# Optimization experiments

Measured on AMD Instinct MI355X. Metric: run time of the kernel, lower is better.

## Reference

```python
import jax, jax.numpy as jnp
import numpy as np

EPS = 1e-5
HEADS = 8  # heads kwarg of TransformerDecoder


def _ln(x, g, b):
    mu = jnp.mean(x, axis=-1, keepdims=True)
    var = jnp.var(x, axis=-1, keepdims=True)
    return (x - mu) * jax.lax.rsqrt(var + EPS) * g + b


def _expert(params, xt, m, scale):
    """One TransformerDecoder expert (BIT-style): per layer, PreNorm2 cross-attn + residual,
    then PreNorm FeedForward + residual. xt: (B,S,D), m: (B,Nt,D)."""
    an_g, an_b, wq, wk, wv, wo, wo_b, fn_g, fn_b, w1, b1, w2, b2 = params
    L = an_g.shape[0]
    B, S, D = xt.shape
    Nt = m.shape[1]
    for l in range(L):
        xn = _ln(xt, an_g[l], an_b[l])
        mn = _ln(m, an_g[l], an_b[l])  # PreNorm2 norms both streams with the same LN
        q = (xn @ wq[l]).reshape(B, S, HEADS, -1)
        k = (mn @ wk[l]).reshape(B, Nt, HEADS, -1)
        v = (mn @ wv[l]).reshape(B, Nt, HEADS, -1)
        attn = jax.nn.softmax(jnp.einsum('bihd,bjhd->bhij', q, k) * scale, axis=-1)
        o = jnp.einsum('bhij,bjhd->bihd', attn, v).reshape(B, S, -1)
        xt = xt + o @ wo[l] + wo_b[l]
        h = _ln(xt, fn_g[l], fn_b[l])
        xt = xt + jax.nn.gelu(h @ w1[l] + b1[l], approximate=False) @ w2[l] + b2[l]
    return xt


def setup_inputs():
    key = jax.random.key(0)
    ks = iter(jax.random.split(key, 40))
    B, C, H, W = 4, 128, 64, 64
    D, INNER, FF, P, L, NT = 256, 512, 1024, 4, 2, 8
    r = lambda shape, s=1.0: jax.random.normal(next(ks), shape, jnp.float32) * s
    return {
        'x': r((B, C, H, W)),
        'm': r((B, NT, D)),
        'proj_w': r((C, D), 0.05), 'proj_b': r((D,), 0.02),
        'lnp_g': jnp.ones((D,), jnp.float32), 'lnp_b': jnp.zeros((D,), jnp.float32),
        'sq_w': r((D, D), 0.05), 'sq_b': r((D,), 0.02),
        'sk_w': r((D, D), 0.05), 'sk_b': r((D,), 0.02),
        'sv_w': r((D, 1), 0.05), 'sv_b': r((1,), 0.02),
        'an_g': jnp.ones((P, L, D), jnp.float32), 'an_b': jnp.zeros((P, L, D), jnp.float32),
        'wq': r((P, L, D, INNER), 0.05), 'wk': r((P, L, D, INNER), 0.05), 'wv': r((P, L, D, INNER), 0.05),
        'wo': r((P, L, INNER, D), 0.05), 'wo_b': r((P, L, D), 0.02),
        'fn_g': jnp.ones((P, L, D), jnp.float32), 'fn_b': jnp.zeros((P, L, D), jnp.float32),
        'w1': r((P, L, D, FF), 0.05), 'b1': r((P, L, FF), 0.02),
        'w2': r((P, L, FF, D), 0.05), 'b2': r((P, L, D), 0.02),
        'fln_g': jnp.ones((D,), jnp.float32), 'fln_b': jnp.zeros((D,), jnp.float32),
    }


def reference(x, m, proj_w, proj_b, lnp_g, lnp_b, sq_w, sq_b, sk_w, sk_b, sv_w, sv_b,
              an_g, an_b, wq, wk, wv, wo, wo_b, fn_g, fn_b, w1, b1, w2, b2, fln_g, fln_b):
    B, C, H, W = x.shape
    D = proj_w.shape[1]
    # 1x1 conv -> flatten(2).transpose(1,2): row-major (h,w) tokens
    tokens = jnp.einsum('bchw,cd->bhwd', x, proj_w).reshape(B, H * W, D) + proj_b
    tokens = _ln(tokens, lnp_g, lnp_b)
    # TokenScorer: cross-attention importance scores, v projects to scalar
    q = tokens @ sq_w + sq_b
    k = m @ sk_w + sk_b
    v = m @ sv_w + sv_b  # (B, Nt, 1)
    aw = jax.nn.softmax(jnp.einsum('bnd,bmd->bnm', q, k) / jnp.sqrt(jnp.float32(D)), axis=-1)
    scores = jnp.einsum('bnm,bmo->bno', aw, v)[..., 0]  # (B, N)
    P = an_g.shape[0]
    N = tokens.shape[1]
    S = N // P
    # descending sort of token scores
    idx = jnp.argsort(-scores, axis=1)  # (B, N)
    pscores = jnp.take_along_axis(scores, idx, axis=1).reshape(B, P, S).mean(-1)  # (B, P)
    pw = jax.nn.softmax(pscores, axis=1)  # (B, P)
    # gather tokens per partition: (P, B, S, D)
    gathered = jnp.take_along_axis(tokens, idx[..., None], axis=1).reshape(B, P, S, D).transpose(1, 0, 2, 3)
    scale = 1.0 / jnp.sqrt(jnp.float32(D))  # Cross_Attention scale = dim ** -0.5
    params = (an_g, an_b, wq, wk, wv, wo, wo_b, fn_g, fn_b, w1, b1, w2, b2)
    proc = jax.vmap(lambda pr, xt: _expert(pr, xt, m, scale))(params, gathered)  # (P, B, S, D)
    proc = proc * pw.T[:, :, None, None]
    flat = proc.transpose(1, 0, 2, 3).reshape(B, N, D)
    # scatter back into original token order (idx is a permutation)
    out = jnp.zeros_like(tokens).at[jnp.arange(B)[:, None], idx].set(flat)
    return _ln(out, fln_g, fln_b)
```

## Files before the change

### kernel.cpp

```cpp
#include <hip/hip_runtime.h>
#include <hip/hip_bf16.h>
#include <math.h>

#define BB 4
#define CC 128
#define NN 4096
#define DD 256
#define INNER 512
#define FFD 1024
#define PP 4
#define LL 2
#define NT 8
#define SS 1024
#define SCALE 0.0625f

typedef __attribute__((ext_vector_type(8))) short bf16x8;
typedef __attribute__((ext_vector_type(8))) short short8;
typedef __attribute__((ext_vector_type(4))) short short4v;
typedef __attribute__((ext_vector_type(4))) float f32x4;

#define GLD_LDS16(g, l) __builtin_amdgcn_global_load_lds( \
    (const __attribute__((address_space(1))) void*)(g), \
    (__attribute__((address_space(3))) void*)(l), 16, 0, 0)

template<int NW>
__device__ inline float block_sum(float v, float* sbuf){
  #pragma unroll
  for (int mk=32; mk; mk>>=1) v += __shfl_xor(v, mk);
  int w = threadIdx.x>>6;
  if ((threadIdx.x&63)==0) sbuf[w]=v;
  __syncthreads();
  float r = 0.f;
  #pragma unroll
  for (int k=0;k<NW;k++) r += sbuf[k];
  __syncthreads();
  return r;
}

__device__ inline unsigned short bf16bits(float v){
  __hip_bfloat16 t = __float2bfloat16(v);
  unsigned short u;
  __builtin_memcpy(&u, &t, 2);
  return u;
}
__device__ inline float bf2f(unsigned short u){
  unsigned int x = ((unsigned int)u)<<16;
  float f;
  __builtin_memcpy(&f, &x, 4);
  return f;
}

__device__ inline float gelu_f(float x){
  float z  = x * 0.70710678118654752440f;
  float az = fabsf(z);
  float t  = 1.0f / (1.0f + 0.3275911f*az);
  float y  = t*(0.254829592f + t*(-0.284496736f + t*(1.421413741f +
             t*(-1.453152027f + t*1.061405429f))));
  float erfv = 1.0f - y*__expf(-az*az);
  erfv = (z < 0.0f) ? -erfv : erfv;
  return 0.5f*x*(1.0f+erfv);
}

__global__ __launch_bounds__(256) void scorer_kernel(
    const float* __restrict__ m, const float* __restrict__ sk_w,
    const float* __restrict__ sk_b, const float* __restrict__ sv_w,
    const float* __restrict__ sv_b, const float* __restrict__ sq_w,
    const float* __restrict__ sq_b,
    float* __restrict__ kk2, float* __restrict__ kb, float* __restrict__ vsc)
{
  __shared__ float ms[256];
  __shared__ float ks[256];
  __shared__ float sbuf[4];
  int bj = blockIdx.x;
  int tid = threadIdx.x;
  ms[tid] = m[bj*DD + tid];
  __syncthreads();
  float acc=0.f;
  #pragma unroll 8
  for(int c=0;c<DD;c++) acc = fmaf(ms[c], sk_w[c*DD + tid], acc);
  ks[tid] = acc + sk_b[tid];
  float sv = block_sum<4>(ms[tid]*sv_w[tid], sbuf);
  if(tid==0) vsc[bj] = sv + sv_b[0];
  __syncthreads();
  const float* wr = sq_w + (long)tid*DD;
  float a2 = 0.f;
  #pragma unroll 4
  for (int c=0; c<DD; c+=4){
    float4 wvv = *(const float4*)(wr + c);
    a2 = fmaf(wvv.x, ks[c+0], fmaf(wvv.y, ks[c+1], fmaf(wvv.z, ks[c+2], fmaf(wvv.w, ks[c+3], a2))));
  }
  kk2[bj*DD + tid] = a2;
  float kbv = block_sum<4>(sq_b[tid]*ks[tid], sbuf);
  if (tid==0) kb[bj] = kbv;
}

__global__ __launch_bounds__(256) void proj_prep_kernel(
    const float* __restrict__ x, const float* __restrict__ proj_w,
    const float* __restrict__ proj_b, const float* __restrict__ lnp_g,
    const float* __restrict__ lnp_b, const float* __restrict__ kk2,
    const float* __restrict__ kb, const float* __restrict__ vsc,
    float* __restrict__ tokens, float* __restrict__ scores,
    int* __restrict__ rank, long long* __restrict__ psumsI,
    const float* __restrict__ m, const float* __restrict__ an_g,
    const float* __restrict__ an_b, const float* __restrict__ wk,
    const float* __restrict__ wv, float* __restrict__ kvk,
    float* __restrict__ kvv,
    const float* __restrict__ wq, const float* __restrict__ w1,
    const float* __restrict__ w2,
    __hip_bfloat16* __restrict__ wqT, __hip_bfloat16* __restrict__ w1T,
    __hip_bfloat16* __restrict__ w2T)
{
  __shared__ union {
    struct {
      float ys[16][260];
      float kj[8][260];
      float kbs[8], vs[8], mu_s[16], rs_s[16];
      float lg[16][8];
    } pr;
    struct { float t[64][65]; } wc;
    struct { float mn[256]; float sbuf[4]; } kv;
  } sm;
  int z = blockIdx.x;
  int tid = threadIdx.x;

  if (z < 256){
    float* mn = sm.kv.mn;
    float* sbuf = sm.kv.sbuf;
    int idx = z;
    int j = idx & 7, b = (idx>>3)&3, pl = idx>>5;
    float v = m[(b*NT+j)*DD + tid];
    float s = block_sum<4>(v, sbuf);
    float mu = s*(1.0f/256.0f);
    float dv = v-mu;
    float q = block_sum<4>(dv*dv, sbuf);
    float rs = rsqrtf(q*(1.0f/256.0f)+1e-5f);
    mn[tid] = dv*rs*an_g[pl*DD+tid] + an_b[pl*DD+tid];
    __syncthreads();
    float ka0=0.f, va0=0.f, ka1=0.f, va1=0.f;
    const float* wkb = wk + (long)pl*DD*INNER;
    const float* wvb = wv + (long)pl*DD*INNER;
    #pragma unroll 8
    for (int c=0;c<DD;c++){
      float mc = mn[c];
      const float* wkr = wkb + (long)c*INNER;
      const float* wvr = wvb + (long)c*INNER;
      ka0 = fmaf(mc, wkr[tid], ka0);
      ka1 = fmaf(mc, wkr[tid+256], ka1);
      va0 = fmaf(mc, wvr[tid], va0);
      va1 = fmaf(mc, wvr[tid+256], va1);
    }
    long off = ((long)pl*BB + b)*(NT*INNER) + j*INNER;
    kvk[off+tid]=ka0; kvk[off+tid+256]=ka1;
    kvv[off+tid]=va0; kvv[off+tid+256]=va1;
  } else if (z < 1536){
    int z2 = z - 256;
    const float* src; __hip_bfloat16* dst; int K, N, rel;
    if (z2 < 256)      { src=wq; dst=wqT; K=DD;   N=INNER; rel=z2; }
    else if (z2 < 768) { src=w1; dst=w1T; K=DD;   N=FFD;   rel=z2-256; }
    else               { src=w2; dst=w2T; K=FFD;  N=DD;    rel=z2-768; }
    int tn = N>>6, tk = K>>6, per = tn*tk;
    int pl = rel/per, r2 = rel%per;
    int n0 = (r2%tn)*64, k0 = (r2/tn)*64;
    float (*t)[65] = sm.wc.t;
    #pragma unroll
    for (int i=0;i<4;i++){
      int idx = i*256+tid;
      int kk = idx>>4, n4 = idx&15;
      float4 v = *(const float4*)&src[((long)pl*K + k0+kk)*N + n0 + n4*4];
      t[kk][n4*4+0]=v.x; t[kk][n4*4+1]=v.y; t[kk][n4*4+2]=v.z; t[kk][n4*4+3]=v.w;
    }
    __syncthreads();
    #pragma unroll
    for (int i=0;i<4;i++){
      int idx = i*256+tid;
      int nn = idx>>4, k4 = idx&15;
      short4v o;
      o[0] = (short)bf16bits(t[k4*4+0][nn]);
      o[1] = (short)bf16bits(t[k4*4+1][nn]);
      o[2] = (short)bf16bits(t[k4*4+2][nn]);
      o[3] = (short)bf16bits(t[k4*4+3][nn]);
      *(short4v*)&dst[((long)pl*N + n0+nn)*K + k0 + k4*4] = o;
    }
  } else {
    int zz = z - 1536;
    int b  = zz >> 8;
    int n0 = (zz & 255) * 16;
    if (tid < 16) rank[b*NN + n0 + tid] = 0;
    if (zz == 0 && tid < 16) psumsI[tid] = 0;
    float (*ys)[260] = sm.pr.ys;
    float (*kj)[260] = sm.pr.kj;
    float* kbs = sm.pr.kbs; float* vs = sm.pr.vs;
    float* mu_s = sm.pr.mu_s; float* rs_s = sm.pr.rs_s;
    float (*lg)[8] = sm.pr.lg;
    #pragma unroll
    for (int i=0;i<8;i++){
      int idx = i*256 + tid;
      int r = idx >> 8, c = idx & 255;
      kj[r][c] = kk2[(b*NT + r)*DD + c];
    }
    if (tid < 8){ kbs[tid] = kb[b*NT+tid]; vs[tid] = vsc[b*NT+tid]; }
    float acc[16];
    #pragma unroll
    for (int t=0;t<16;t++) acc[t]=0.f;
    const float* xb = x + (long)(b*CC)*NN + n0;
    for (int c0=0;c0<CC;c0+=4){
      float w0 = proj_w[(c0+0)*DD + tid];
      float w1_ = proj_w[(c0+1)*DD + tid];
      float w2_ = proj_w[(c0+2)*DD + tid];
      float w3_ = proj_w[(c0+3)*DD + tid];
      const float* x0 = xb + (long)(c0+0)*NN;
      const float* x1 = xb + (long)(c0+1)*NN;
      const float* x2 = xb + (long)(c0+2)*NN;
      const float* x3 = xb + (long)(c0+3)*NN;
      #pragma unroll
      for (int t=0;t<16;t++){
        acc[t] = fmaf(x0[t],w0,fmaf(x1[t],w1_,fmaf(x2[t],w2_,fmaf(x3[t],w3_,acc[t]))));
      }
    }
    float pb = proj_b[tid];
    #pragma unroll
    for (int t=0;t<16;t++) ys[t][tid] = acc[t] + pb;
    __syncthreads();
    int w = tid>>6, lane = tid&63;
    for (int k=0;k<4;k++){
      int t = w*4+k;
      float s = ys[t][lane] + ys[t][lane+64] + ys[t][lane+128] + ys[t][lane+192];
      #pragma unroll
      for (int mk=32; mk; mk>>=1) s += __shfl_xor(s, mk);
      float mu = s*(1.0f/256.0f);
      float d0=ys[t][lane]-mu, d1=ys[t][lane+64]-mu, d2=ys[t][lane+128]-mu, d3=ys[t][lane+192]-mu;
      float q = d0*d0+d1*d1+d2*d2+d3*d3;
      #pragma unroll
      for (int mk=32; mk; mk>>=1) q += __shfl_xor(q, mk);
      if (lane==0){ mu_s[t]=mu; rs_s[t]=rsqrtf(q*(1.0f/256.0f)+1e-5f); }
    }
    __syncthreads();
    float g = lnp_g[tid], be = lnp_b[tid];
    #pragma unroll
    for (int t=0;t<16;t++){
      float nv = (ys[t][tid]-mu_s[t])*rs_s[t]*g + be;
      tokens[((long)(b*NN + n0 + t))*DD + tid] = nv;
      ys[t][tid] = nv;
    }
    __syncthreads();
    if (tid < 128){
      int t = tid>>3, j = tid&7;
      float a2 = 0.f;
      for (int c0=0;c0<DD;c0+=4){
        float4 tv = *(const float4*)&ys[t][c0];
        float4 kv2 = *(const float4*)&kj[j][c0];
        a2 = fmaf(tv.x,kv2.x,fmaf(tv.y,kv2.y,fmaf(tv.z,kv2.z,fmaf(tv.w,kv2.w,a2))));
      }
      lg[t][j] = (a2 + kbs[j]) * SCALE;
    }
    __syncthreads();
    if (tid < 16){
      float mx=-1e30f;
      #pragma unroll
      for(int j=0;j<NT;j++) mx=fmaxf(mx,lg[tid][j]);
      float s=0.f, sc=0.f;
      #pragma unroll
      for(int j=0;j<NT;j++){ float e=__expf(lg[tid][j]-mx); s+=e; sc+=e*vs[j]; }
      scores[b*NN + n0 + tid] = sc/s;
    }
  }
}

__global__ __launch_bounds__(256) void rank_qkvwo_kernel(
    const float* __restrict__ scores, int* __restrict__ rank,
    const float* __restrict__ kvk, const float* __restrict__ kvv,
    const __hip_bfloat16* __restrict__ wqT, const float* __restrict__ wo,
    __hip_bfloat16* __restrict__ qkBuf, __hip_bfloat16* __restrict__ vwoT)
{
  __shared__ union {
    struct { float ss[256]; } rk;
    struct { float kL[8][64]; float vL[8][64]; } qv;
  } sm;
  int z = blockIdx.x;
  if (z >= 256){
    int zz = z - 256;
    int b  = zz >> 8;
    int it = (zz >> 4) & 15;
    int jt = zz & 15;
    int i = it*256 + threadIdx.x;
    float si = scores[b*NN + i];
    sm.rk.ss[threadIdx.x] = scores[b*NN + jt*256 + threadIdx.x];
    __syncthreads();
    int jbase = jt*256;
    int cnt = 0;
    #pragma unroll 4
    for (int j=0;j<256;j++){
      float sj = sm.rk.ss[j];
      cnt += (sj > si) || (sj == si && (jbase+j) < i);
    }
    atomicAdd(&rank[b*NN+i], cnt);
  } else {
    int zz = z;
    int z3 = zz>>3, h = zz&7;
    int l = z3>>4, g = z3&15;
    int b = g>>2, p = g&3;
    int pl = p*LL + l;
    int c = threadIdx.x;
    float (*kL)[64] = sm.qv.kL;
    float (*vL)[64] = sm.qv.vL;
    {
      int j0 = c>>6, d0 = c&63;
      long off = ((long)pl*BB + b)*(NT*INNER) + h*64 + d0;
      kL[j0][d0]   = kvk[off + j0*INNER];
      vL[j0][d0]   = kvv[off + j0*INNER];
      kL[j0+4][d0] = kvk[off + (j0+4)*INNER];
      vL[j0+4][d0] = kvv[off + (j0+4)*INNER];
    }
    __syncthreads();
    float qa[8] = {0,0,0,0,0,0,0,0};
    float va[8] = {0,0,0,0,0,0,0,0};
    const __hip_bfloat16* wqp = wqT + ((long)pl*INNER + h*64)*DD + c;
    const float* wop = wo + ((long)pl*INNER + h*64)*DD + c;
    #pragma unroll 4
    for (int d=0; d<64; d++){
      float wqv = bf2f(*(const unsigned short*)(wqp + (long)d*DD));
      float wov = wop[(long)d*DD];
      #pragma unroll
      for (int j=0;j<8;j++){
        qa[j] = fmaf(kL[j][d], wqv, qa[j]);
        va[j] = fmaf(vL[j][d], wov, va[j]);
      }
    }
    __hip_bfloat16* qkg = qkBuf + (long)z3*64*256;
    __hip_bfloat16* vwg = vwoT + (long)z3*256*64;
    #pragma unroll
    for (int j=0;j<8;j++)
      qkg[(h*8+j)*256 + c] = __float2bfloat16(qa[j]*SCALE);
    short8 o;
    #pragma unroll
    for (int j=0;j<8;j++) o[j] = (short)bf16bits(va[j]);
    *(short8*)(vwg + c*64 + h*8) = o;
  }
}

__global__ __launch_bounds__(256) void rank_finalize_kernel(
    const int* __restrict__ rank, const float* __restrict__ scores,
    int* __restrict__ cidx, long long* __restrict__ psumsI)
{
  __shared__ unsigned long long bins[PP];
  if (threadIdx.x < PP) bins[threadIdx.x] = 0ull;
  __syncthreads();
  int b = blockIdx.x >> 4;
  int i = (blockIdx.x & 15)*256 + threadIdx.x;
  int rk = rank[b*NN + i];
  int p = rk >> 10;
  cidx[(b*PP + p)*SS + (rk & (SS-1))] = i;
  long long iv = (long long)llrintf(scores[b*NN + i] * 268435456.0f);
  atomicAdd(&bins[p], (unsigned long long)iv);
  __syncthreads();
  if (threadIdx.x < PP)
    atomicAdd((unsigned long long*)&psumsI[b*PP + threadIdx.x], bins[threadIdx.x]);
}

__global__ __launch_bounds__(256) void gather_ln_kernel(
    const float* __restrict__ tokens, const int* __restrict__ cidx,
    float* __restrict__ Xc, __hip_bfloat16* __restrict__ Y,
    const float* __restrict__ gamma, const float* __restrict__ beta)
{
  long slot = (long)blockIdx.x*8 + (threadIdx.x>>5);
  int l32 = threadIdx.x & 31;
  int b = (int)(slot >> 12);
  int p = (int)((slot>>10)&3);
  int i = cidx[slot];
  const float* src = tokens + ((long)b*NN + i)*DD + l32*8;
  float4 v0 = *(const float4*)src;
  float4 v1 = *(const float4*)(src+4);
  *(float4*)(Xc + slot*DD + l32*8) = v0;
  *(float4*)(Xc + slot*DD + l32*8 + 4) = v1;
  float s = v0.x+v0.y+v0.z+v0.w+v1.x+v1.y+v1.z+v1.w;
  #pragma unroll
  for (int mk=16; mk; mk>>=1) s += __shfl_xor(s, mk);
  float mu = s*(1.0f/256.0f);
  float vv[8] = {v0.x,v0.y,v0.z,v0.w,v1.x,v1.y,v1.z,v1.w};
  float q = 0.f;
  #pragma unroll
  for (int k=0;k<8;k++){ float d = vv[k]-mu; q += d*d; }
  #pragma unroll
  for (int mk=16; mk; mk>>=1) q += __shfl_xor(q, mk);
  float rs = rsqrtf(q*(1.0f/256.0f)+1e-5f);
  short8 o;
  #pragma unroll
  for (int k=0;k<8;k++){
    int d = l32*8+k;
    o[k] = (short)bf16bits((vv[k]-mu)*rs*gamma[p*(LL*DD)+d]+beta[p*(LL*DD)+d]);
  }
  *(short8*)(Y + slot*DD + l32*8) = o;
}

__global__ __launch_bounds__(256) void ff1_gemm(
    const __hip_bfloat16* __restrict__ A, long astride,
    const __hip_bfloat16* __restrict__ BT, long bpstride,
    const float* __restrict__ bias, int bias_pstride,
    __hip_bfloat16* __restrict__ C, int ldc, long cstride)
{
  int g = blockIdx.z;
  int p = g & 3;
  const __hip_bfloat16* Ag = A  + (long)g*astride + (long)blockIdx.x*128*DD;
  const __hip_bfloat16* Bg = BT + (long)p*bpstride + (long)blockIdx.y*128*DD;
  const float* biasg = bias + (long)p*bias_pstride;

  __shared__ __align__(16) __hip_bfloat16 Asm[4][128*64];
  __shared__ __align__(16) __hip_bfloat16 Bsm[4][128*64];

  int tid = threadIdx.x;
  int w = tid>>6, lane = tid&63;
  int wr = w>>1, wc = w&1;
  int lr = lane>>4, lc = lane&15;
  int ldsbase = tid & ~63;

  #pragma unroll
  for (int c=0;c<4;c++){
    #pragma unroll
    for (int i=0;i<4;i++){
      int seg = i*256 + tid;
      int r = seg>>3, sl = seg&7;
      int sg = sl ^ (r&7);
      GLD_LDS16(Ag + (long)r*DD + c*64 + sg*8, &Asm[c][(i*256 + ldsbase)*8]);
      GLD_LDS16(Bg + (long)r*DD + c*64 + sg*8, &Bsm[c][(i*256 + ldsbase)*8]);
    }
  }
  asm volatile("s_waitcnt vmcnt(0)" ::: "memory");
  __syncthreads();

  f32x4 acc[4][4] = {};
  #pragma unroll
  for (int t=0;t<4;t++){
    #pragma unroll
    for (int kc=0;kc<2;kc++){
      bf16x8 af[4], bfr[4];
      #pragma unroll
      for (int mi=0;mi<4;mi++){
        int r = wr*64 + mi*16 + lc;
        int s = kc*4 + lr;
        af[mi] = *(const bf16x8*)(&Asm[t][r*64 + (s ^ (r&7))*8]);
      }
      #pragma unroll
      for (int ni=0;ni<4;ni++){
        int r = wc*64 + ni*16 + lc;
        int s = kc*4 + lr;
        bfr[ni] = *(const bf16x8*)(&Bsm[t][r*64 + (s ^ (r&7))*8]);
      }
      #pragma unroll
      for (int mi=0;mi<4;mi++)
        #pragma unroll
        for (int ni=0;ni<4;ni++)
          acc[mi][ni] = __builtin_amdgcn_mfma_f32_16x16x32_bf16(af[mi], bfr[ni], acc[mi][ni], 0, 0, 0);
    }
  }

  __hip_bfloat16* Cg = C + (long)g*cstride;
  #pragma unroll
  for (int ni=0;ni<4;ni++){
    int col = blockIdx.y*128 + wc*64 + ni*16 + lc;
    float bv = biasg[col];
    #pragma unroll
    for (int mi=0;mi<4;mi++){
      int row = blockIdx.x*128 + wr*64 + mi*16 + lr*4;
      #pragma unroll
      for (int j=0;j<4;j++){
        float v = acc[mi][ni][j] + bv;
        v = gelu_f(v);
        Cg[(long)(row+j)*ldc + col] = __float2bfloat16(v);
      }
    }
  }
}

template<bool LAST>
__global__ __launch_bounds__(256) void ff2_fused_kernel(
    const __hip_bfloat16* __restrict__ F,
    const __hip_bfloat16* __restrict__ w2l,
    const float* __restrict__ b2l,
    float* __restrict__ Xc,
    const float* __restrict__ g_ln,
    const float* __restrict__ b_ln,
    __hip_bfloat16* __restrict__ actOut,
    const int* __restrict__ cidx,
    const long long* __restrict__ psumsI,
    float* __restrict__ out)
{
  int rb = blockIdx.x;
  int g  = blockIdx.y;
  int p  = g & 3;
  const __hip_bfloat16* Ag = F + ((long)g*SS + rb*32)*FFD;
  const __hip_bfloat16* Bg = w2l + (long)p*((long)LL*DD*FFD);

  __shared__ __align__(16) __hip_bfloat16 As[2][32*64];
  __shared__ __align__(16) __hip_bfloat16 Bs[2][256*64];

  int tid = threadIdx.x;
  int w = tid>>6, lane = tid&63;
  int lr = lane>>4, lc = lane&15;
  int ldsbase = tid & ~63;

  const __hip_bfloat16* aseg;
  const __hip_bfloat16* bseg[8];
  {
    int seg = tid;
    int r = seg>>3, sl = seg&7;
    aseg = Ag + (long)r*FFD + (sl ^ (r&7))*8;
  }
  #pragma unroll
  for (int i=0;i<8;i++){
    int seg = i*256 + tid;
    int r = seg>>3, sl = seg&7;
    bseg[i] = Bg + (long)r*FFD + (sl ^ (r&7))*8;
  }

  f32x4 acc[2][4] = {};

  #define STAGE2(buf) do { \
    GLD_LDS16(aseg, &As[buf][ldsbase*8]); \
    _Pragma("unroll") \
    for (int i_=0;i_<8;i_++) \
      GLD_LDS16(bseg[i_], &Bs[buf][(i_*256 + ldsbase)*8]); \
    aseg += 64; \
    _Pragma("unroll") \
    for (int i_=0;i_<8;i_++) bseg[i_] += 64; \
  } while(0)

  STAGE2(0);
  asm volatile("s_waitcnt vmcnt(0)" ::: "memory");
  __syncthreads();

  for (int t=0; t<16; t++){
    int cur = t & 1;
    if (t+1 < 16) STAGE2(cur^1);
    #pragma unroll
    for (int kc=0;kc<2;kc++){
      bf16x8 af[2], bfr[4];
      #pragma unroll
      for (int mi=0;mi<2;mi++){
        int r = mi*16 + lc;
        int s = kc*4 + lr;
        af[mi] = *(const bf16x8*)(&As[cur][r*64 + (s ^ (r&7))*8]);
      }
      #pragma unroll
      for (int ni=0;ni<4;ni++){
        int c = w*64 + ni*16 + lc;
        int s = kc*4 + lr;
        bfr[ni] = *(const bf16x8*)(&Bs[cur][c*64 + (s ^ (c&7))*8]);
      }
      #pragma unroll
      for (int mi=0;mi<2;mi++)
        #pragma unroll
        for (int ni=0;ni<4;ni++)
          acc[mi][ni] = __builtin_amdgcn_mfma_f32_16x16x32_bf16(af[mi], bfr[ni], acc[mi][ni], 0, 0, 0);
    }
    if (t+1 < 16) asm volatile("s_waitcnt vmcnt(0)" ::: "memory");
    __syncthreads();
  }
  #undef STAGE2

  __syncthreads();
  float* pfl = (float*)&As[0][0];
  float* pfq = (float*)&As[0][0] + 128;
  float* Xg = Xc + (long)g*SS*DD + (long)rb*32*DD;

  float pwv = 1.0f;
  if (LAST){
    int b = g>>2;
    float ps[4];
    #pragma unroll
    for (int p2=0;p2<4;p2++)
      ps[p2] = (float)((double)psumsI[b*PP+p2] * (1.0/268435456.0/1024.0));
    float mxp = fmaxf(fmaxf(ps[0],ps[1]),fmaxf(ps[2],ps[3]));
    float e0=__expf(ps[0]-mxp), e1=__expf(ps[1]-mxp), e2=__expf(ps[2]-mxp), e3=__expf(ps[3]-mxp);
    float es = e0+e1+e2+e3;
    float ev = (p==0)?e0:(p==1)?e1:(p==2)?e2:e3;
    pwv = ev/es;
  }

  float srow[2][4], qrow[2][4];
  #pragma unroll
  for (int mi=0;mi<2;mi++)
    #pragma unroll
    for (int j=0;j<4;j++){ srow[mi][j]=0.f; qrow[mi][j]=0.f; }
  #pragma unroll
  for (int ni=0;ni<4;ni++){
    int col = w*64 + ni*16 + lc;
    float bv = b2l[p*(LL*DD) + col];
    #pragma unroll
    for (int mi=0;mi<2;mi++){
      int row = mi*16 + lr*4;
      #pragma unroll
      for (int j=0;j<4;j++){
        float v = Xg[(long)(row+j)*DD + col] + acc[mi][ni][j] + bv;
        if (!LAST) Xg[(long)(row+j)*DD + col] = v;
        if (LAST) v *= pwv;
        acc[mi][ni][j] = v;
        srow[mi][j] += v;
        qrow[mi][j] += v*v;
      }
    }
  }
  #pragma unroll
  for (int mi=0;mi<2;mi++)
    #pragma unroll
    for (int j=0;j<4;j++){
      float s2=srow[mi][j], q2=qrow[mi][j];
      s2 += __shfl_xor(s2,1); q2 += __shfl_xor(q2,1);
      s2 += __shfl_xor(s2,2); q2 += __shfl_xor(q2,2);
      s2 += __shfl_xor(s2,4); q2 += __shfl_xor(q2,4);
      s2 += __shfl_xor(s2,8); q2 += __shfl_xor(q2,8);
      srow[mi][j]=s2; qrow[mi][j]=q2;
    }
  if (lc==0){
    #pragma unroll
    for (int mi=0;mi<2;mi++)
      #pragma unroll
      for (int j=0;j<4;j++){
        int row = mi*16 + lr*4 + j;
        pfl[w*32+row] = srow[mi][j];
        pfq[w*32+row] = qrow[mi][j];
      }
  }
  __syncthreads();

  if (!LAST){
    __hip_bfloat16* Ya = actOut + ((long)g*SS + rb*32)*DD;
    const float* fg = g_ln + p*(LL*DD);
    const float* fb = b_ln + p*(LL*DD);
    #pragma unroll
    for (int mi=0;mi<2;mi++){
      #pragma unroll
      for (int j=0;j<4;j++){
        int row = mi*16 + lr*4 + j;
        float S = pfl[row] + pfl[32+row] + pfl[64+row] + pfl[96+row];
        float Q = pfq[row] + pfq[32+row] + pfq[64+row] + pfq[96+row];
        float mu = S*(1.0f/256.0f);
        float var = Q*(1.0f/256.0f) - mu*mu;
        float rs2 = rsqrtf(var + 1e-5f);
        #pragma unroll
        for (int ni=0;ni<4;ni++){
          int col = w*64 + ni*16 + lc;
          Ya[(long)row*DD + col] =
              __float2bfloat16((acc[mi][ni][j]-mu)*rs2*fg[col]+fb[col]);
        }
      }
    }
  } else {
    int b = g>>2;
    #pragma unroll
    for (int mi=0;mi<2;mi++){
      #pragma unroll
      for (int j=0;j<4;j++){
        int row = mi*16 + lr*4 + j;
        long slot = (long)g*SS + rb*32 + row;
        int i = cidx[slot];
        float S = pfl[row] + pfl[32+row] + pfl[64+row] + pfl[96+row];
        float Q = pfq[row] + pfq[32+row] + pfq[64+row] + pfq[96+row];
        float mu = S*(1.0f/256.0f);
        float var = Q*(1.0f/256.0f) - mu*mu;
        float rs2 = rsqrtf(var + 1e-5f);
        float* op = out + ((long)b*NN + i)*DD;
        #pragma unroll
        for (int ni=0;ni<4;ni++){
          int col = w*64 + ni*16 + lc;
          op[col] = (acc[mi][ni][j]-mu)*rs2*g_ln[col]+b_ln[col];
        }
      }
    }
  }
}

__global__ __launch_bounds__(256) void fused_attn_kernel(
    const __hip_bfloat16* __restrict__ actA,
    const __hip_bfloat16* __restrict__ qk,
    const __hip_bfloat16* __restrict__ vwo,
    const float* __restrict__ wo_bl,
    const float* __restrict__ fn_gl,
    const float* __restrict__ fn_bl,
    float* __restrict__ Xc,
    __hip_bfloat16* __restrict__ actOut)
{
  int rb = blockIdx.x;
  int g  = blockIdx.y;
  int p  = g & 3;
  const __hip_bfloat16* Ag = actA + ((long)g*SS + rb*32)*DD;
  const __hip_bfloat16* Qg = qk  + (long)g*64*256;
  const __hip_bfloat16* Vg = vwo + (long)g*256*64;

  __shared__ __align__(16) __hip_bfloat16 sm[24576];
  int tid = threadIdx.x;
  int w = tid>>6, lane = tid&63;
  int lr = lane>>4, lc = lane&15;
  int ldsbase = tid & ~63;

  #pragma unroll
  for (int i=0;i<8;i++){
    int seg = i*256 + tid;
    int r = seg>>5, sl = seg&31;
    int sg = sl ^ (r&7);
    GLD_LDS16(Qg + (long)r*256 + sg*8, &sm[8192 + (i*256 + ldsbase)*8]);
  }
  {
    int r = tid>>3, sl = tid&7;
    int sg = sl ^ (r&7);
    GLD_LDS16(Ag + (long)r*DD + sg*8, &sm[0 + ldsbase*8]);
  }
  asm volatile("s_waitcnt vmcnt(0)" ::: "memory");
  __syncthreads();

  f32x4 acc1[2] = {};
  for (int t=0; t<4; t++){
    int cur = t&1;
    if (t+1 < 4){
      int r = tid>>3, sl = tid&7;
      int sg = sl ^ (r&7);
      GLD_LDS16(Ag + (long)r*DD + (t+1)*64 + sg*8,
                &sm[(cur^1)*2048 + ldsbase*8]);
    }
    #pragma unroll
    for (int kc=0;kc<2;kc++){
      int r = (w&1)*16 + lc;
      int s = kc*4 + lr;
      bf16x8 af = *(const bf16x8*)(&sm[cur*2048 + r*64 + (s ^ (r&7))*8]);
      #pragma unroll
      for (int ni=0;ni<2;ni++){
        int rb_ = (w>>1)*32 + ni*16 + lc;
        int sb = t*8 + kc*4 + lr;
        bf16x8 bfr = *(const bf16x8*)(&sm[8192 + rb_*256 + (sb ^ (rb_&7))*8]);
        acc1[ni] = __builtin_amdgcn_mfma_f32_16x16x32_bf16(af, bfr, acc1[ni], 0, 0, 0);
      }
    }
    if (t+1 < 4) asm volatile("s_waitcnt vmcnt(0)" ::: "memory");
    __syncthreads();
  }

  #pragma unroll
  for (int i=0;i<8;i++){
    int seg = i*256 + tid;
    int r = seg>>3, sl = seg&7;
    int sg = sl ^ (r&7);
    GLD_LDS16(Vg + (long)r*64 + sg*8, &sm[8192 + (i*256 + ldsbase)*8]);
  }

  float pv[2][4];
  #pragma unroll
  for (int ni=0;ni<2;ni++){
    #pragma unroll
    for (int j=0;j<4;j++){
      float v = acc1[ni][j];
      float mx = v;
      mx = fmaxf(mx, __shfl_xor(mx,1));
      mx = fmaxf(mx, __shfl_xor(mx,2));
      mx = fmaxf(mx, __shfl_xor(mx,4));
      float e = __expf(v - mx);
      float ssum = e;
      ssum += __shfl_xor(ssum,1);
      ssum += __shfl_xor(ssum,2);
      ssum += __shfl_xor(ssum,4);
      pv[ni][j] = e / ssum;
    }
  }
  #pragma unroll
  for (int ni=0;ni<2;ni++){
    #pragma unroll
    for (int j=0;j<4;j++){
      int row = (w&1)*16 + lr*4 + j;
      int col = (w>>1)*32 + ni*16 + lc;
      int s = col>>3, e = col&7;
      sm[row*64 + ((s ^ (row&7))<<3) + e] = __float2bfloat16(pv[ni][j]);
    }
  }
  asm volatile("s_waitcnt vmcnt(0)" ::: "memory");
  __syncthreads();

  f32x4 acc2[2][4] = {};
  #pragma unroll
  for (int kc=0;kc<2;kc++){
    bf16x8 af[2], bfr[4];
    #pragma unroll
    for (int mi=0;mi<2;mi++){
      int r = mi*16 + lc;
      int s = kc*4 + lr;
      af[mi] = *(const bf16x8*)(&sm[r*64 + (s ^ (r&7))*8]);
    }
    #pragma unroll
    for (int ni=0;ni<4;ni++){
      int rb_ = w*64 + ni*16 + lc;
      int s = kc*4 + lr;
      bfr[ni] = *(const bf16x8*)(&sm[8192 + rb_*64 + (s ^ (rb_&7))*8]);
    }
    #pragma unroll
    for (int mi=0;mi<2;mi++)
      #pragma unroll
      for (int ni=0;ni<4;ni++)
        acc2[mi][ni] = __builtin_amdgcn_mfma_f32_16x16x32_bf16(af[mi], bfr[ni], acc2[mi][ni], 0, 0, 0);
  }

  __syncthreads();
  float* pfl = (float*)sm;
  float* pfq = (float*)sm + 128;
  float* Xg = Xc + (long)g*SS*DD + (long)rb*32*DD;
  float srow[2][4], qrow[2][4];
  #pragma unroll
  for (int mi=0;mi<2;mi++)
    #pragma unroll
    for (int j=0;j<4;j++){ srow[mi][j]=0.f; qrow[mi][j]=0.f; }
  #pragma unroll
  for (int ni=0;ni<4;ni++){
    int col = w*64 + ni*16 + lc;
    float bv = wo_bl[p*(LL*DD) + col];
    #pragma unroll
    for (int mi=0;mi<2;mi++){
      int row = mi*16 + lr*4;
      #pragma unroll
      for (int j=0;j<4;j++){
        float v = Xg[(long)(row+j)*DD + col] + acc2[mi][ni][j] + bv;
        Xg[(long)(row+j)*DD + col] = v;
        acc2[mi][ni][j] = v;
        srow[mi][j] += v;
        qrow[mi][j] += v*v;
      }
    }
  }
  #pragma unroll
  for (int mi=0;mi<2;mi++)
    #pragma unroll
    for (int j=0;j<4;j++){
      float s2=srow[mi][j], q2=qrow[mi][j];
      s2 += __shfl_xor(s2,1); q2 += __shfl_xor(q2,1);
      s2 += __shfl_xor(s2,2); q2 += __shfl_xor(q2,2);
      s2 += __shfl_xor(s2,4); q2 += __shfl_xor(q2,4);
      s2 += __shfl_xor(s2,8); q2 += __shfl_xor(q2,8);
      srow[mi][j]=s2; qrow[mi][j]=q2;
    }
  if (lc==0){
    #pragma unroll
    for (int mi=0;mi<2;mi++)
      #pragma unroll
      for (int j=0;j<4;j++){
        int row = mi*16 + lr*4 + j;
        pfl[w*32+row] = srow[mi][j];
        pfq[w*32+row] = qrow[mi][j];
      }
  }
  __syncthreads();
  __hip_bfloat16* Ya = actOut + ((long)g*SS + rb*32)*DD;
  const float* fg = fn_gl + p*(LL*DD);
  const float* fb = fn_bl + p*(LL*DD);
  #pragma unroll
  for (int mi=0;mi<2;mi++){
    #pragma unroll
    for (int j=0;j<4;j++){
      int row = mi*16 + lr*4 + j;
      float S = pfl[row] + pfl[32+row] + pfl[64+row] + pfl[96+row];
      float Q = pfq[row] + pfq[32+row] + pfq[64+row] + pfq[96+row];
      float mu = S*(1.0f/256.0f);
      float var = Q*(1.0f/256.0f) - mu*mu;
      float rs2 = rsqrtf(var + 1e-5f);
      #pragma unroll
      for (int ni=0;ni<4;ni++){
        int col = w*64 + ni*16 + lc;
        Ya[(long)row*DD + col] =
            __float2bfloat16((acc2[mi][ni][j]-mu)*rs2*fg[col]+fb[col]);
      }
    }
  }
}

extern "C" void kernel_launch(void* const* d_in, const int* in_sizes, int n_in,
                              void* d_out, int out_size, void* d_ws, size_t ws_size,
                              hipStream_t stream)
{
  (void)in_sizes; (void)n_in; (void)out_size; (void)ws_size;
  const float* x     =(const float*)d_in[0];
  const float* m     =(const float*)d_in[1];
  const float* proj_w=(const float*)d_in[2];
  const float* proj_b=(const float*)d_in[3];
  const float* lnp_g =(const float*)d_in[4];
  const float* lnp_b =(const float*)d_in[5];
  const float* sq_w  =(const float*)d_in[6];
  const float* sq_b  =(const float*)d_in[7];
  const float* sk_w  =(const float*)d_in[8];
  const float* sk_b  =(const float*)d_in[9];
  const float* sv_w  =(const float*)d_in[10];
  const float* sv_b  =(const float*)d_in[11];
  const float* an_g  =(const float*)d_in[12];
  const float* an_b  =(const float*)d_in[13];
  const float* wq    =(const float*)d_in[14];
  const float* wk    =(const float*)d_in[15];
  const float* wv    =(const float*)d_in[16];
  const float* wo    =(const float*)d_in[17];
  const float* wo_b  =(const float*)d_in[18];
  const float* fn_g  =(const float*)d_in[19];
  const float* fn_b  =(const float*)d_in[20];
  const float* w1    =(const float*)d_in[21];
  const float* b1    =(const float*)d_in[22];
  const float* w2    =(const float*)d_in[23];
  const float* b2    =(const float*)d_in[24];
  const float* fln_g =(const float*)d_in[25];
  const float* fln_b =(const float*)d_in[26];
  float* out = (float*)d_out;

  float* ws = (float*)d_ws;
  float* tokens  = ws;  ws += 4194304;
  ws += 4194304;
  float* Xc      = ws;  ws += 4194304;
  float* actAf   = ws;  ws += 2097152;
  float* wqTf    = ws;  ws += 524288;
  float* w1Tf    = ws;  ws += 1048576;
  float* w2Tf    = ws;  ws += 1048576;
  float* qkBf    = ws;  ws += 262144;
  float* vwoTf   = ws;  ws += 262144;
  float* kvk     = ws;  ws += 131072;
  float* kvv     = ws;  ws += 131072;
  float* kk2     = ws;  ws += 8192;
  float* kb      = ws;  ws += 32;
  float* vsc     = ws;  ws += 64;
  float* scores  = ws;  ws += 16384;
  long long* psumsI = (long long*)ws;  ws += 32;
  int* rank      = (int*)ws;  ws += 16384;
  int* cidx      = (int*)ws;  ws += 16384;

  __hip_bfloat16* actA  = (__hip_bfloat16*)actAf;
  __hip_bfloat16* actF  = (__hip_bfloat16*)tokens;
  __hip_bfloat16* wqT   = (__hip_bfloat16*)wqTf;
  __hip_bfloat16* w1T   = (__hip_bfloat16*)w1Tf;
  __hip_bfloat16* w2T   = (__hip_bfloat16*)w2Tf;
  __hip_bfloat16* qkBuf = (__hip_bfloat16*)qkBf;
  __hip_bfloat16* vwoT  = (__hip_bfloat16*)vwoTf;

  scorer_kernel<<<32,256,0,stream>>>(m, sk_w, sk_b, sv_w, sv_b, sq_w, sq_b,
                                     kk2, kb, vsc);
  proj_prep_kernel<<<2560,256,0,stream>>>(
      x, proj_w, proj_b, lnp_g, lnp_b, kk2, kb, vsc,
      tokens, scores, rank, psumsI,
      m, an_g, an_b, wk, wv, kvk, kvv,
      wq, w1, w2, wqT, w1T, w2T);
  rank_qkvwo_kernel<<<1280,256,0,stream>>>(scores, rank, kvk, kvv, wqT, wo,
                                           qkBuf, vwoT);
  rank_finalize_kernel<<<64,256,0,stream>>>(rank, scores, cidx, psumsI);
  gather_ln_kernel<<<2048,256,0,stream>>>(tokens, cidx, Xc, actA, an_g, an_b);

  fused_attn_kernel<<<dim3(32,16),256,0,stream>>>(
      actA, qkBuf, vwoT, wo_b, fn_g, fn_b, Xc, actA);
  ff1_gemm<<<dim3(8,8,16),256,0,stream>>>(
      actA, (long)SS*DD, w1T, (long)LL*FFD*DD,
      b1, LL*FFD, actF, FFD, (long)SS*FFD);
  ff2_fused_kernel<false><<<dim3(32,16),256,0,stream>>>(
      actF, w2T, b2, Xc, an_g + DD, an_b + DD, actA,
      nullptr, nullptr, nullptr);
  fused_attn_kernel<<<dim3(32,16),256,0,stream>>>(
      actA, qkBuf + (long)16*64*256, vwoT + (long)16*256*64,
      wo_b + DD, fn_g + DD, fn_b + DD, Xc, actA);
  ff1_gemm<<<dim3(8,8,16),256,0,stream>>>(
      actA, (long)SS*DD, w1T + (long)FFD*DD, (long)LL*FFD*DD,
      b1 + FFD, LL*FFD, actF, FFD, (long)SS*FFD);
  ff2_fused_kernel<true><<<dim3(32,16),256,0,stream>>>(
      actF, w2T + (long)DD*FFD, b2 + DD, Xc, fln_g, fln_b, nullptr,
      cidx, psumsI, out);
}
```

Baseline: 230.6 us.

## Shrink FF1 GEMM tile to 128x64 and double-buffer K-chunk loads

The FF1 GEMM output tile shrinks from 128x128 to 128x64, which doubles the grid to 2048 blocks. The shared-memory footprint falls from 128KB to 48KB. Instead of loading all four K chunks up front, the kernel now double-buffers 64-wide K chunks so the next chunk's global-to-LDS load overlaps MFMA work on the current one. The goal is higher occupancy and less load latency, at the cost of an extra barrier per K step and lower per-block data reuse.

Measured after the change: 216.7 us. -6.0%, faster.

```diff
diff --git a/kernel.cpp b/kernel.cpp
--- a/kernel.cpp
+++ b/kernel.cpp
@@ -401,66 +401,88 @@
   int g = blockIdx.z;
   int p = g & 3;
   const __hip_bfloat16* Ag = A  + (long)g*astride + (long)blockIdx.x*128*DD;
-  const __hip_bfloat16* Bg = BT + (long)p*bpstride + (long)blockIdx.y*128*DD;
+  const __hip_bfloat16* Bg = BT + (long)p*bpstride + (long)blockIdx.y*64*DD;
   const float* biasg = bias + (long)p*bias_pstride;
 
-  __shared__ __align__(16) __hip_bfloat16 Asm[4][128*64];
-  __shared__ __align__(16) __hip_bfloat16 Bsm[4][128*64];
+  __shared__ __align__(16) __hip_bfloat16 Asm[2][128*64];
+  __shared__ __align__(16) __hip_bfloat16 Bsm[2][64*64];
 
   int tid = threadIdx.x;
   int w = tid>>6, lane = tid&63;
-  int wr = w>>1, wc = w&1;
   int lr = lane>>4, lc = lane&15;
   int ldsbase = tid & ~63;
 
-  #pragma unroll
-  for (int c=0;c<4;c++){
-    #pragma unroll
-    for (int i=0;i<4;i++){
-      int seg = i*256 + tid;
-      int r = seg>>3, sl = seg&7;
-      int sg = sl ^ (r&7);
-      GLD_LDS16(Ag + (long)r*DD + c*64 + sg*8, &Asm[c][(i*256 + ldsbase)*8]);
-      GLD_LDS16(Bg + (long)r*DD + c*64 + sg*8, &Bsm[c][(i*256 + ldsbase)*8]);
-    }
-  }
+  const __hip_bfloat16* aseg[4];
+  const __hip_bfloat16* bseg[2];
+  #pragma unroll
+  for (int i=0;i<4;i++){
+    int seg = i*256 + tid;
+    int r = seg>>3, sl = seg&7;
+    aseg[i] = Ag + (long)r*DD + (sl ^ (r&7))*8;
+  }
+  #pragma unroll
+  for (int i=0;i<2;i++){
+    int seg = i*256 + tid;
+    int r = seg>>3, sl = seg&7;
+    bseg[i] = Bg + (long)r*DD + (sl ^ (r&7))*8;
+  }
+
+  f32x4 acc[2][4] = {};
+
+  #define STAGE1(buf) do { \
+    _Pragma("unroll") \
+    for (int i_=0;i_<4;i_++) \
+      GLD_LDS16(aseg[i_], &Asm[buf][(i_*256 + ldsbase)*8]); \
+    _Pragma("unroll") \
+    for (int i_=0;i_<2;i_++) \
+      GLD_LDS16(bseg[i_], &Bsm[buf][(i_*256 + ldsbase)*8]); \
+    _Pragma("unroll") \
+    for (int i_=0;i_<4;i_++) aseg[i_] += 64; \
+    _Pragma("unroll") \
+    for (int i_=0;i_<2;i_++) bseg[i_] += 64; \
+  } while(0)
+
+  STAGE1(0);
   asm volatile("s_waitcnt vmcnt(0)" ::: "memory");
   __syncthreads();
 
-  f32x4 acc[4][4] = {};
-  #pragma unroll
-  for (int t=0;t<4;t++){
+  for (int t=0; t<4; t++){
+    int cur = t & 1;
+    if (t+1 < 4) STAGE1(cur^1);
     #pragma unroll
     for (int kc=0;kc<2;kc++){
-      bf16x8 af[4], bfr[4];
-      #pragma unroll
-      for (int mi=0;mi<4;mi++){
-        int r = wr*64 + mi*16 + lc;
+      bf16x8 af[2], bfr[4];
+      #pragma unroll
+      for (int mi=0;mi<2;mi++){
+        int r = w*32 + mi*16 + lc;
         int s = kc*4 + lr;
-        af[mi] = *(const bf16x8*)(&Asm[t][r*64 + (s ^ (r&7))*8]);
+        af[mi] = *(const bf16x8*)(&Asm[cur][r*64 + (s ^ (r&7))*8]);
       }
       #pragma unroll
       for (int ni=0;ni<4;ni++){
-        int r = wc*64 + ni*16 + lc;
+        int r = ni*16 + lc;
         int s = kc*4 + lr;
-        bfr[ni] = *(const bf16x8*)(&Bsm[t][r*64 + (s ^ (r&7))*8]);
-      }
-      #pragma unroll
-      for (int mi=0;mi<4;mi++)
+        bfr[ni] = *(const bf16x8*)(&Bsm[cur][r*64 + (s ^ (r&7))*8]);
+      }
+      #pragma unroll
+      for (int mi=0;mi<2;mi++)
         #pragma unroll
         for (int ni=0;ni<4;ni++)
           acc[mi][ni] = __builtin_amdgcn_mfma_f32_16x16x32_bf16(af[mi], bfr[ni], acc[mi][ni], 0, 0, 0);
     }
-  }
+    if (t+1 < 4) asm volatile("s_waitcnt vmcnt(0)" ::: "memory");
+    __syncthreads();
+  }
+  #undef STAGE1
 
   __hip_bfloat16* Cg = C + (long)g*cstride;
   #pragma unroll
   for (int ni=0;ni<4;ni++){
-    int col = blockIdx.y*128 + wc*64 + ni*16 + lc;
+    int col = blockIdx.y*64 + ni*16 + lc;
     float bv = biasg[col];
     #pragma unroll
-    for (int mi=0;mi<4;mi++){
-      int row = blockIdx.x*128 + wr*64 + mi*16 + lr*4;
+    for (int mi=0;mi<2;mi++){
+      int row = blockIdx.x*128 + w*32 + mi*16 + lr*4;
       #pragma unroll
       for (int j=0;j<4;j++){
         float v = acc[mi][ni][j] + bv;
@@ -942,7 +964,7 @@
 
   fused_attn_kernel<<<dim3(32,16),256,0,stream>>>(
       actA, qkBuf, vwoT, wo_b, fn_g, fn_b, Xc, actA);
-  ff1_gemm<<<dim3(8,8,16),256,0,stream>>>(
+  ff1_gemm<<<dim3(8,16,16),256,0,stream>>>(
       actA, (long)SS*DD, w1T, (long)LL*FFD*DD,
       b1, LL*FFD, actF, FFD, (long)SS*FFD);
   ff2_fused_kernel<false><<<dim3(32,16),256,0,stream>>>(
@@ -951,7 +973,7 @@
   fused_attn_kernel<<<dim3(32,16),256,0,stream>>>(
       actA, qkBuf + (long)16*64*256, vwoT + (long)16*256*64,
       wo_b + DD, fn_g + DD, fn_b + DD, Xc, actA);
-  ff1_gemm<<<dim3(8,8,16),256,0,stream>>>(
+  ff1_gemm<<<dim3(8,16,16),256,0,stream>>>(
       actA, (long)SS*DD, w1T + (long)FFD*DD, (long)LL*FFD*DD,
       b1 + FFD, LL*FFD, actF, FFD, (long)SS*FFD);
   ff2_fused_kernel<true><<<dim3(32,16),256,0,stream>>>(
```
